# Optimization experiments

Measured on AMD Instinct MI355X. Metric: run time of the kernel, lower is better.

Reference implementation:

```python
import jax, jax.numpy as jnp
import numpy as np

B, S, D = 2, 2048, 1024
H = 16
HD = D // H  # 64
ROPE_BASE = 10000.0


def rotate_half(x):
    x1, x2 = jnp.split(x, 2, axis=-1)
    return jnp.concatenate((-x2, x1), axis=-1)


def rope_cos_sin(seq_len, dim, dtype):
    inv_freq = 1.0 / (ROPE_BASE ** (jnp.arange(0, dim, 2, dtype=jnp.float32) / dim))
    t = jnp.arange(seq_len, dtype=jnp.float32)
    freqs = jnp.einsum('i,j->ij', t, inv_freq)          # [S, dim/2]
    emb = jnp.concatenate((freqs, freqs), axis=-1)      # [S, dim]
    return jnp.cos(emb).astype(dtype), jnp.sin(emb).astype(dtype)


def setup_inputs() -> dict:
    key = jax.random.key(0)
    ks = jax.random.split(key, 5)
    std = 0.02
    return {
        'x': jax.random.normal(ks[0], (B, S, D), dtype=jnp.float32),
        'wq': jax.random.normal(ks[1], (D, D), dtype=jnp.float32) * std,
        'wk': jax.random.normal(ks[2], (D, D), dtype=jnp.float32) * std,
        'wv': jax.random.normal(ks[3], (D, D), dtype=jnp.float32) * std,
        'wo': jax.random.normal(ks[4], (D, D), dtype=jnp.float32) * std,
    }


def reference(x, wq, wk, wv, wo):
    b, s, d = x.shape
    # Q/K/V projections (nn.Linear: x @ W.T)
    q = jnp.einsum('bsd,ed->bse', x, wq).reshape(b, s, H, HD).transpose(0, 2, 1, 3)
    k = jnp.einsum('bsd,ed->bse', x, wk).reshape(b, s, H, HD).transpose(0, 2, 1, 3)
    v = jnp.einsum('bsd,ed->bse', x, wv).reshape(b, s, H, HD).transpose(0, 2, 1, 3)
    # RoPE
    cos, sin = rope_cos_sin(s, HD, x.dtype)  # [s, HD]
    cos = cos[None, None]  # [1,1,s,HD]
    sin = sin[None, None]
    q = q * cos + rotate_half(q) * sin
    k = k * cos + rotate_half(k) * sin
    # Causal SDPA
    scale = HD ** -0.5
    scores = jnp.einsum('bhqd,bhkd->bhqk', q, k) * scale
    causal = jnp.tril(jnp.ones((s, s), dtype=bool))
    scores = jnp.where(causal[None, None], scores, jnp.finfo(scores.dtype).min)
    attn = jax.nn.softmax(scores, axis=-1)
    out = jnp.einsum('bhqk,bhkd->bhqd', attn, v)
    out = out.transpose(0, 2, 1, 3).reshape(b, s, d)
    return jnp.einsum('bsd,ed->bse', out, wo)
```

## Files before the change

### kernel.cpp

```cpp
#include <hip/hip_runtime.h>
#include <hip/hip_bf16.h>
#include <cstdint>
#include <cstddef>

#define BDIM 2
#define SDIM 2048
#define DDIM 1024
#define HN   16
#define HDIM 64

using bf16 = __bf16;
typedef __attribute__((ext_vector_type(8))) __bf16 bf16x8;
typedef __attribute__((ext_vector_type(4))) __bf16 bf16x4;
typedef __attribute__((ext_vector_type(4))) float  f32x4;

#define MFMA16(a, b, c) __builtin_amdgcn_mfma_f32_16x16x32_bf16((a), (b), (c), 0, 0, 0)

#define ASYNC16(g, l)                                                          \
  __builtin_amdgcn_global_load_lds(                                            \
      (const __attribute__((address_space(1))) void*)(g),                      \
      (__attribute__((address_space(3))) void*)(l), 16, 0, 0)

#define QSCALE 0.1803368801111204f

__global__ __launch_bounds__(256) void cvt_bf16(const float* __restrict__ src,
                                                bf16* __restrict__ dst, int n4) {
  int i = blockIdx.x * 256 + threadIdx.x;
  if (i < n4) {
    float4 v = ((const float4*)src)[i];
    bf16x4 o = {(__bf16)v.x, (__bf16)v.y, (__bf16)v.z, (__bf16)v.w};
    *(bf16x4*)(dst + (size_t)i * 4) = o;
  }
}

struct Ptr4 { const float* p[4]; };
__global__ __launch_bounds__(256) void cvt_w(Ptr4 srcs, bf16* __restrict__ dst) {
  const int seg = blockIdx.y;
  const float* src = srcs.p[seg];
  int i = blockIdx.x * 256 + threadIdx.x;
  float4 v = ((const float4*)src)[i];
  bf16x4 o = {(__bf16)v.x, (__bf16)v.y, (__bf16)v.z, (__bf16)v.w};
  *(bf16x4*)(dst + (size_t)seg * (DDIM * DDIM) + (size_t)i * 4) = o;
}

__global__ __launch_bounds__(256) void rope_table(float* __restrict__ cosT,
                                                  float* __restrict__ sinT) {
  int i = blockIdx.x * 256 + threadIdx.x;
  int s = i >> 5, j = i & 31;
  float inv = powf(10000.f, -(float)j * (1.f / 32.f));
  float a = (float)s * inv;
  float sn, c;
  sincosf(a, &sn, &c);
  cosT[s * 64 + j]      = c;
  cosT[s * 64 + j + 32] = c;
  sinT[s * 64 + j]      = sn;
  sinT[s * 64 + j + 32] = sn;
}

__global__ __launch_bounds__(256) void fixup_qk(bf16* __restrict__ q,
                                                bf16* __restrict__ k,
                                                const float* __restrict__ cosT,
                                                const float* __restrict__ sinT) {
  const int bh = blockIdx.y;
  const int s = blockIdx.x * 32 + (threadIdx.x >> 3);
  const int j0 = (threadIdx.x & 7) * 4;
  const size_t base = ((size_t)bh * SDIM + s) * HDIM;
  const float4 c4 = *(const float4*)(cosT + s * 64 + j0);
  const float4 s4 = *(const float4*)(sinT + s * 64 + j0);
  const float cc[4] = {c4.x, c4.y, c4.z, c4.w};
  const float ss[4] = {s4.x, s4.y, s4.z, s4.w};

  bf16x4 qlo = *(bf16x4*)(q + base + j0);
  bf16x4 qhi = *(bf16x4*)(q + base + j0 + 32);
  bf16x4 klo = *(bf16x4*)(k + base + j0);
  bf16x4 khi = *(bf16x4*)(k + base + j0 + 32);
  bf16x4 rql, rqh, rkl, rkh;
#pragma unroll
  for (int e = 0; e < 4; ++e) {
    float a = (float)qlo[e], b = (float)qhi[e];
    rql[e] = (__bf16)((a * cc[e] - b * ss[e]) * QSCALE);
    rqh[e] = (__bf16)((b * cc[e] + a * ss[e]) * QSCALE);
    a = (float)klo[e]; b = (float)khi[e];
    rkl[e] = (__bf16)(a * cc[e] - b * ss[e]);
    rkh[e] = (__bf16)(b * cc[e] + a * ss[e]);
  }
  *(bf16x4*)(q + base + j0)      = rql;
  *(bf16x4*)(q + base + j0 + 32) = rqh;
  *(bf16x4*)(k + base + j0)      = rkl;
  *(bf16x4*)(k + base + j0 + 32) = rkh;
}

__global__ __launch_bounds__(512) void gemm_qkv(const bf16* __restrict__ A,
                                                const bf16* __restrict__ Bw,
                                                bf16* __restrict__ C0,
                                                bf16* __restrict__ Vt) {
  constexpr int K = 1024;
  __shared__ __align__(16) bf16 As[2][256 * 64];
  __shared__ __align__(16) bf16 Bs[2][256 * 64];
  const int tid = threadIdx.x;
  const int l = tid & 63, w = tid >> 6;
  const int wr = w >> 2, wc = w & 3;
  const int lr = l & 15, lg = l >> 4;

  const int bid = blockIdx.x;
  const int swb = (bid & 7) * 24 + (bid >> 3);
  const int mt = swb & 15, nt = swb >> 4;
  const int bm = mt * 256, bn = nt * 256;

  f32x4 acc[8][4] = {};

  auto stage = [&](int buf, int k0) {
#pragma unroll
    for (int i = 0; i < 4; ++i) {
      int lin = i * 4096 + tid * 8;
      int row = lin >> 6, col = lin & 63;
      ASYNC16(A + (size_t)(bm + row) * K + (k0 + col), As[buf] + lin);
      ASYNC16(Bw + (size_t)(bn + row) * K + (k0 + col), Bs[buf] + lin);
    }
  };

  stage(0, 0);
  asm volatile("s_waitcnt vmcnt(0)" ::: "memory");
  __builtin_amdgcn_s_barrier();

  for (int k = 0; k < 16; ++k) {
    const int cur = k & 1;
    if (k < 15) {
      stage(cur ^ 1, (k + 1) * 64);
      asm volatile("s_waitcnt vmcnt(8)" ::: "memory");
    } else {
      asm volatile("s_waitcnt vmcnt(0)" ::: "memory");
    }
    __builtin_amdgcn_sched_barrier(0);
    __builtin_amdgcn_s_barrier();

    const bf16* Ab = As[cur];
    const bf16* Bb = Bs[cur];
#pragma unroll
    for (int kc = 0; kc < 2; ++kc) {
      bf16x8 a[8], b[4];
#pragma unroll
      for (int m = 0; m < 8; ++m)
        a[m] = *(const bf16x8*)(Ab + (wr * 128 + m * 16 + lr) * 64 + kc * 32 + lg * 8);
#pragma unroll
      for (int n = 0; n < 4; ++n)
        b[n] = *(const bf16x8*)(Bb + (wc * 64 + n * 16 + lr) * 64 + kc * 32 + lg * 8);
      __builtin_amdgcn_s_setprio(1);
#pragma unroll
      for (int m = 0; m < 8; ++m)
#pragma unroll
        for (int n = 0; n < 4; ++n)
          acc[m][n] = MFMA16(a[m], b[n], acc[m][n]);
      __builtin_amdgcn_s_setprio(0);
    }
    __builtin_amdgcn_sched_barrier(0);
    __builtin_amdgcn_s_barrier();
    __builtin_amdgcn_sched_barrier(0);
  }

  const int z = bn >> 10;
  const int bcol = bn & 1023;
  if (z < 2) {
    bf16* C = C0 + (size_t)z * ((size_t)BDIM * SDIM * DDIM);
#pragma unroll
    for (int m = 0; m < 8; ++m) {
      const int row0 = bm + wr * 128 + m * 16 + lg * 4;
      const int bb = row0 >> 11, s = row0 & (SDIM - 1);
#pragma unroll
      for (int n = 0; n < 4; ++n) {
        const int h = (bcol >> 6) + wc;
        const int hd = n * 16 + lr;
        const size_t base = ((size_t)(bb * HN + h) * SDIM + s) * HDIM + hd;
#pragma unroll
        for (int r = 0; r < 4; ++r)
          C[base + (size_t)r * HDIM] = (__bf16)acc[m][n][r];
      }
    }
  } else {
#pragma unroll
    for (int m = 0; m < 8; ++m) {
      const int row0 = bm + wr * 128 + m * 16 + lg * 4;
      const int bb = row0 >> 11, s0 = row0 & (SDIM - 1);
#pragma unroll
      for (int n = 0; n < 4; ++n) {
        const int h = (bcol >> 6) + wc;
        const int hd = n * 16 + lr;
        bf16x4 pv = {(__bf16)acc[m][n][0], (__bf16)acc[m][n][1],
                     (__bf16)acc[m][n][2], (__bf16)acc[m][n][3]};
        *(bf16x4*)(Vt + ((size_t)(bb * HN + h) * HDIM + hd) * SDIM + s0) = pv;
      }
    }
  }
}

__global__ __launch_bounds__(256) void gemm_out(const bf16* __restrict__ A,
                                                const bf16* __restrict__ Bw,
                                                float* __restrict__ C) {
  constexpr int K = 1024;
  __shared__ __align__(16) bf16 As[128 * 64];
  __shared__ __align__(16) bf16 Bs[128 * 64];
  const int tid = threadIdx.x;
  const int l = tid & 63, w = tid >> 6;
  const int wr = w >> 1, wc = w & 1;
  const int lr = l & 15, lg = l >> 4;
  const int bm = blockIdx.y * 128;
  const int bn = blockIdx.x * 128;

  f32x4 acc[4][4] = {};

  for (int k0 = 0; k0 < K; k0 += 64) {
    __syncthreads();
#pragma unroll
    for (int i = 0; i < 4; ++i) {
      int idx = i * 2048 + tid * 8;
      int row = idx >> 6, col = idx & 63;
      ASYNC16(A + (size_t)(bm + row) * K + (k0 + col), As + idx);
      ASYNC16(Bw + (size_t)(bn + row) * K + (k0 + col), Bs + idx);
    }
    __syncthreads();
#pragma unroll
    for (int c = 0; c < 2; ++c) {
      bf16x8 af[4], bfr[4];
#pragma unroll
      for (int m = 0; m < 4; ++m)
        af[m] = *(const bf16x8*)(As + (wr * 64 + m * 16 + lr) * 64 + c * 32 + lg * 8);
#pragma unroll
      for (int n = 0; n < 4; ++n)
        bfr[n] = *(const bf16x8*)(Bs + (wc * 64 + n * 16 + lr) * 64 + c * 32 + lg * 8);
      __builtin_amdgcn_s_setprio(1);
#pragma unroll
      for (int m = 0; m < 4; ++m)
#pragma unroll
        for (int n = 0; n < 4; ++n)
          acc[m][n] = MFMA16(af[m], bfr[n], acc[m][n]);
      __builtin_amdgcn_s_setprio(0);
    }
  }

#pragma unroll
  for (int m = 0; m < 4; ++m)
#pragma unroll
    for (int n = 0; n < 4; ++n)
#pragma unroll
      for (int r = 0; r < 4; ++r) {
        int row = bm + wr * 64 + m * 16 + lg * 4 + r;
        int col = bn + wc * 64 + n * 16 + lr;
        C[(size_t)row * DDIM + col] = acc[m][n][r];
      }
}

__global__ __launch_bounds__(512) void attn_fwd(const bf16* __restrict__ qg,
                                                const bf16* __restrict__ kg,
                                                const bf16* __restrict__ vtg,
                                                bf16* __restrict__ og) {
  __shared__ __align__(16) bf16 Sl[2][3][4096];
  __shared__ __align__(16) bf16 Pl[8][1024];

  const int tid = threadIdx.x;
  const int l = tid & 63, w = tid >> 6;
  const int g = w >> 2, wg = w & 3;
  const int lr = l & 15, lg = l >> 4;
  const int bh = blockIdx.x;
  const int qt = 31 - blockIdx.y;
  const int q0 = qt * 64;
  const size_t hb = (size_t)bh * SDIM * HDIM;
  const bf16* Q  = qg + hb;
  const bf16* Kp = kg + hb;
  const bf16* Vp = vtg + hb;
  const int b = bh >> 4, h = bh & 15;
  bf16* Pw = &Pl[w][0];
  const int swz = lr & 7;

  const int mm0 = 2 * wg, mm1 = 2 * wg + 1;
  const int f0 = mm0 & 3, c0 = mm0 >> 2;
  const int f1 = mm1 & 3, c1 = mm1 >> 2;
  const int lo0 = mm0 * 512 + l * 8;
  const int lo1 = mm1 * 512 + l * 8;
  bf16* const SlG = &Sl[g][0][0];

  bf16x8 qf[2];
#pragma unroll
  for (int c = 0; c < 2; ++c)
    qf[c] = *(const bf16x8*)(Q + (size_t)(q0 + wg * 16 + lr) * HDIM + c * 32 + lg * 8);

  f32x4 o[4] = {};
  float m = -3e38f, lsum = 0.f;

  const int ng   = (qt >= g) ? ((qt - g) >> 1) + 1 : 0;
  const int smax = (qt >> 1) + 1;

  const bf16* kN0 = Kp + (size_t)(f0 * 16 + lr) * HDIM + c0 * 32 + lg * 8 + (size_t)g * 64 * HDIM;
  const bf16* kN1 = Kp + (size_t)(f1 * 16 + lr) * HDIM + c1 * 32 + lg * 8 + (size_t)g * 64 * HDIM;
  const bf16* vN0 = Vp + (size_t)(f0 * 16 + lr) * SDIM + c0 * 32 + lg * 8 + g * 64;
  const bf16* vN1 = Vp + (size_t)(f1 * 16 + lr) * SDIM + c1 * 32 + lg * 8 + g * 64;

  if (ng > 0) {
    ASYNC16(kN0, SlG + 0 * 4096 + lo0); kN0 += 128 * HDIM;
    ASYNC16(kN1, SlG + 0 * 4096 + lo1); kN1 += 128 * HDIM;
    ASYNC16(vN0, SlG + 1 * 4096 + lo0); vN0 += 128;
    ASYNC16(vN1, SlG + 1 * 4096 + lo1); vN1 += 128;
  }
  __syncthreads();

  int ks = 0, vs = 1;
  for (int s = 0; s < smax; ++s) {
    const int t = 2 * s + g;
    const bool act = (s < ng);
    const int kn = 3 - ks - vs;
    const bool hasNext = act && (s + 1 < ng);

    if (hasNext) {
      ASYNC16(kN0, SlG + kn * 4096 + lo0); kN0 += 128 * HDIM;
      ASYNC16(kN1, SlG + kn * 4096 + lo1); kN1 += 128 * HDIM;
    }

    const bool diag = (t == qt);
    const int fLim = diag ? wg : 3;

    f32x4 sc[4] = {};
    if (act) {
      __builtin_amdgcn_s_setprio(1);
#pragma unroll
      for (int c = 0; c < 2; ++c)
#pragma unroll
        for (int f = 0; f < 4; ++f)
          if (f <= fLim) {
            bf16x8 kfr = *(const bf16x8*)(SlG + ks * 4096 + (c * 4 + f) * 512 + l * 8);
            sc[f] = MFMA16(kfr, qf[c], sc[f]);
          }
      __builtin_amdgcn_s_setprio(0);
    }

    __builtin_amdgcn_s_barrier();
    __builtin_amdgcn_sched_barrier(0);

    if (hasNext) {
      ASYNC16(vN0, SlG + ks * 4096 + lo0); vN0 += 128;
      ASYNC16(vN1, SlG + ks * 4096 + lo1); vN1 += 128;
    }

    if (act) {
      if (diag) {
#pragma unroll
        for (int f = 0; f < 4; ++f)
#pragma unroll
          for (int r = 0; r < 4; ++r) {
            if (f > wg)
              sc[f][r] = -3e38f;
            else if (f == wg)
              sc[f][r] = (lg * 4 + r <= lr) ? sc[f][r] : -3e38f;
          }
      }

      float mxl = -3e38f;
#pragma unroll
      for (int f = 0; f < 4; ++f)
#pragma unroll
        for (int r = 0; r < 4; ++r) mxl = fmaxf(mxl, sc[f][r]);

      if (!__all(mxl - m <= 8.f)) {
        float mx = fmaxf(mxl, __shfl_xor(mxl, 16));
        mx = fmaxf(mx, __shfl_xor(mx, 32));
        float mnew = fmaxf(m, mx);
        float corr = exp2f(m - mnew);
        m = mnew;
        lsum *= corr;
        float cb[4];
#pragma unroll
        for (int r = 0; r < 4; ++r) cb[r] = __shfl(corr, lg * 4 + r);
#pragma unroll
        for (int n = 0; n < 4; ++n)
#pragma unroll
          for (int r = 0; r < 4; ++r) o[n][r] *= cb[r];
      }

      float rs = 0.f;
#pragma unroll
      for (int f = 0; f < 4; ++f) {
        float p0 = exp2f(sc[f][0] - m);
        float p1 = exp2f(sc[f][1] - m);
        float p2 = exp2f(sc[f][2] - m);
        float p3 = exp2f(sc[f][3] - m);
        rs += (p0 + p1) + (p2 + p3);
        bf16x4 pv = {(__bf16)p0, (__bf16)p1, (__bf16)p2, (__bf16)p3};
        const int ch = f * 2 + (lg >> 1);
        *(bf16x4*)(Pw + lr * 64 + ((ch ^ swz) << 3) + (lg & 1) * 4) = pv;
      }
      lsum += rs;

      const int cLim = diag ? (wg >> 1) : 1;
      __builtin_amdgcn_s_setprio(1);
#pragma unroll
      for (int c = 0; c < 2; ++c)
        if (c <= cLim) {
          bf16x8 pf = *(const bf16x8*)(Pw + lr * 64 + (((c * 4 + lg) ^ swz) << 3));
#pragma unroll
          for (int n = 0; n < 4; ++n) {
            bf16x8 vfr = *(const bf16x8*)(SlG + vs * 4096 + (c * 4 + n) * 512 + l * 8);
            o[n] = MFMA16(pf, vfr, o[n]);
          }
        }
      __builtin_amdgcn_s_setprio(0);
    }

    __syncthreads();
    vs = ks;
    ks = kn;
  }

  float* Osh = (float*)&Sl[0][0][0];
  float* Msh = Osh + 4096;
  float* Lsh = Msh + 256;

  if (g == 1) {
    Msh[wg * 64 + l] = m;
    Lsh[wg * 64 + l] = lsum;
#pragma unroll
    for (int n = 0; n < 4; ++n)
#pragma unroll
      for (int r = 0; r < 4; ++r)
        Osh[((wg * 4 + n) * 4 + r) * 64 + l] = o[n][r];
  }
  __syncthreads();

  if (g == 0) {
    float m1 = Msh[wg * 64 + l], l1 = Lsh[wg * 64 + l];
    float mt = fmaxf(m, m1);
    float a0 = exp2f(m - mt), a1 = exp2f(m1 - mt);
    float lt = lsum * a0 + l1 * a1;
    lt += __shfl_xor(lt, 16);
    lt += __shfl_xor(lt, 32);
    float a0b[4], a1b[4], ltb[4];
#pragma unroll
    for (int r = 0; r < 4; ++r) {
      a0b[r] = __shfl(a0, lg * 4 + r);
      a1b[r] = __shfl(a1, lg * 4 + r);
      ltb[r] = __shfl(lt, lg * 4 + r);
    }
#pragma unroll
    for (int r = 0; r < 4; ++r) {
      float rl = 1.f / ltb[r];
      int qr = q0 + 16 * wg + lg * 4 + r;
#pragma unroll
      for (int n = 0; n < 4; ++n) {
        float o1 = Osh[((wg * 4 + n) * 4 + r) * 64 + l];
        og[((size_t)(b * SDIM + qr)) * DDIM + h * HDIM + n * 16 + lr] =
            (__bf16)((o[n][r] * a0b[r] + o1 * a1b[r]) * rl);
      }
    }
  }
}

extern "C" void kernel_launch(void* const* d_in, const int* in_sizes, int n_in,
                              void* d_out, int out_size, void* d_ws, size_t ws_size,
                              hipStream_t stream) {
  const float* x  = (const float*)d_in[0];
  const float* wq = (const float*)d_in[1];
  const float* wk = (const float*)d_in[2];
  const float* wv = (const float*)d_in[3];
  const float* wo = (const float*)d_in[4];

  char* ws = (char*)d_ws;
  const size_t MB = 1024 * 1024;
  bf16* xb   = (bf16*)(ws + 0);
  bf16* wqb  = (bf16*)(ws + 8 * MB);
  bf16* wob  = (bf16*)(ws + 14 * MB);
  bf16* qb   = (bf16*)(ws + 16 * MB);
  bf16* kb   = (bf16*)(ws + 24 * MB);
  bf16* vtb  = (bf16*)(ws + 32 * MB);
  bf16* ob   = (bf16*)(ws + 40 * MB);
  float* cosT = (float*)(ws + 48 * MB);
  float* sinT = (float*)(ws + 49 * MB);

  const int NX = BDIM * SDIM * DDIM;
  const int NW = DDIM * DDIM;

  cvt_bf16<<<NX / 4 / 256, 256, 0, stream>>>(x, xb, NX / 4);
  Ptr4 wsrc{{wq, wk, wv, wo}};
  cvt_w<<<dim3(NW / 4 / 256, 4), 256, 0, stream>>>(wsrc, wqb);
  rope_table<<<(SDIM * 32) / 256, 256, 0, stream>>>(cosT, sinT);
  gemm_qkv<<<192, 512, 0, stream>>>(xb, wqb, qb, vtb);
  fixup_qk<<<dim3(SDIM / 32, 32), 256, 0, stream>>>(qb, kb, cosT, sinT);
  attn_fwd<<<dim3(32, 32), 512, 0, stream>>>(qb, kb, vtb, ob);
  gemm_out<<<dim3(8, 32), 256, 0, stream>>>(ob, wob, (float*)d_out);
}
```

Baseline: 146.9 us.

## Retile QKV GEMM to 128x128 blocks, merge conversion kernels, widen gemm_out blocks

Replaces the double-buffered 256x256 QKV GEMM (192 blocks, 512 threads) with a simpler single-buffered 128x128 tile over a 3D grid (768 blocks, 256 threads), one z-slice per Q/K/V weight. The goal is to fill all compute units, since 192 blocks cannot. The trade is lost load/compute overlap and less data reuse per tile. The input and weight fp32-to-bf16 conversions are fused into one launch, and gemm_out moves to 512 threads with a smaller per-wave tile.

```diff
diff --git a/kernel.cpp b/kernel.cpp
--- a/kernel.cpp
+++ b/kernel.cpp
@@ -23,24 +23,29 @@
 
 #define QSCALE 0.1803368801111204f
 
-__global__ __launch_bounds__(256) void cvt_bf16(const float* __restrict__ src,
-                                                bf16* __restrict__ dst, int n4) {
+struct Ptr5 { const float* p[5]; };
+__global__ __launch_bounds__(256) void cvt_all(Ptr5 srcs, bf16* __restrict__ xb,
+                                               bf16* __restrict__ wb) {
+  const int NX4 = (BDIM * SDIM * DDIM) / 4;
   int i = blockIdx.x * 256 + threadIdx.x;
-  if (i < n4) {
-    float4 v = ((const float4*)src)[i];
-    bf16x4 o = {(__bf16)v.x, (__bf16)v.y, (__bf16)v.z, (__bf16)v.w};
-    *(bf16x4*)(dst + (size_t)i * 4) = o;
-  }
-}
-
-struct Ptr4 { const float* p[4]; };
-__global__ __launch_bounds__(256) void cvt_w(Ptr4 srcs, bf16* __restrict__ dst) {
-  const int seg = blockIdx.y;
-  const float* src = srcs.p[seg];
-  int i = blockIdx.x * 256 + threadIdx.x;
-  float4 v = ((const float4*)src)[i];
+  const float* src;
+  bf16* dst;
+  int j;
+  if (i < NX4) {
+    src = srcs.p[0]; dst = xb; j = i;
+  } else {
+    int k = i - NX4;
+    int seg = k >> 18;
+    j = k & 262143;
+    src = srcs.p[seg + 1];
+    dst = wb + (size_t)seg * (DDIM * DDIM) / 1;
+    dst += 0;
+    j = j;
+    dst = wb + (size_t)seg * (DDIM * DDIM);
+  }
+  float4 v = ((const float4*)src)[j];
   bf16x4 o = {(__bf16)v.x, (__bf16)v.y, (__bf16)v.z, (__bf16)v.w};
-  *(bf16x4*)(dst + (size_t)seg * (DDIM * DDIM) + (size_t)i * 4) = o;
+  *(bf16x4*)(dst + (size_t)j * 4) = o;
 }
 
 __global__ __launch_bounds__(256) void rope_table(float* __restrict__ cosT,
@@ -90,101 +95,75 @@
   *(bf16x4*)(k + base + j0 + 32) = rkh;
 }
 
-__global__ __launch_bounds__(512) void gemm_qkv(const bf16* __restrict__ A,
-                                                const bf16* __restrict__ Bw,
+__global__ __launch_bounds__(256) void gemm_qkv(const bf16* __restrict__ A,
+                                                const bf16* __restrict__ B0,
                                                 bf16* __restrict__ C0,
                                                 bf16* __restrict__ Vt) {
   constexpr int K = 1024;
-  __shared__ __align__(16) bf16 As[2][256 * 64];
-  __shared__ __align__(16) bf16 Bs[2][256 * 64];
+  __shared__ __align__(16) bf16 As[128 * 64];
+  __shared__ __align__(16) bf16 Bs[128 * 64];
   const int tid = threadIdx.x;
   const int l = tid & 63, w = tid >> 6;
-  const int wr = w >> 2, wc = w & 3;
+  const int wr = w >> 1, wc = w & 1;
   const int lr = l & 15, lg = l >> 4;
-
-  const int bid = blockIdx.x;
-  const int swb = (bid & 7) * 24 + (bid >> 3);
-  const int mt = swb & 15, nt = swb >> 4;
-  const int bm = mt * 256, bn = nt * 256;
-
-  f32x4 acc[8][4] = {};
-
-  auto stage = [&](int buf, int k0) {
+  const int bm = blockIdx.y * 128;
+  const int bn = blockIdx.x * 128;
+  const bf16* Bw = B0 + (size_t)blockIdx.z * (1024 * 1024);
+
+  f32x4 acc[4][4] = {};
+
+  for (int k0 = 0; k0 < K; k0 += 64) {
+    __syncthreads();
 #pragma unroll
     for (int i = 0; i < 4; ++i) {
-      int lin = i * 4096 + tid * 8;
-      int row = lin >> 6, col = lin & 63;
-      ASYNC16(A + (size_t)(bm + row) * K + (k0 + col), As[buf] + lin);
-      ASYNC16(Bw + (size_t)(bn + row) * K + (k0 + col), Bs[buf] + lin);
-    }
-  };
-
-  stage(0, 0);
-  asm volatile("s_waitcnt vmcnt(0)" ::: "memory");
-  __builtin_amdgcn_s_barrier();
-
-  for (int k = 0; k < 16; ++k) {
-    const int cur = k & 1;
-    if (k < 15) {
-      stage(cur ^ 1, (k + 1) * 64);
-      asm volatile("s_waitcnt vmcnt(8)" ::: "memory");
-    } else {
-      asm volatile("s_waitcnt vmcnt(0)" ::: "memory");
-    }
-    __builtin_amdgcn_sched_barrier(0);
-    __builtin_amdgcn_s_barrier();
-
-    const bf16* Ab = As[cur];
-    const bf16* Bb = Bs[cur];
-#pragma unroll
-    for (int kc = 0; kc < 2; ++kc) {
-      bf16x8 a[8], b[4];
-#pragma unroll
-      for (int m = 0; m < 8; ++m)
-        a[m] = *(const bf16x8*)(Ab + (wr * 128 + m * 16 + lr) * 64 + kc * 32 + lg * 8);
+      int idx = i * 2048 + tid * 8;
+      int row = idx >> 6, col = idx & 63;
+      ASYNC16(A + (size_t)(bm + row) * K + (k0 + col), As + idx);
+      ASYNC16(Bw + (size_t)(bn + row) * K + (k0 + col), Bs + idx);
+    }
+    __syncthreads();
+#pragma unroll
+    for (int c = 0; c < 2; ++c) {
+      bf16x8 af[4], bfr[4];
+#pragma unroll
+      for (int m = 0; m < 4; ++m)
+        af[m] = *(const bf16x8*)(As + (wr * 64 + m * 16 + lr) * 64 + c * 32 + lg * 8);
 #pragma unroll
       for (int n = 0; n < 4; ++n)
-        b[n] = *(const bf16x8*)(Bb + (wc * 64 + n * 16 + lr) * 64 + kc * 32 + lg * 8);
+        bfr[n] = *(const bf16x8*)(Bs + (wc * 64 + n * 16 + lr) * 64 + c * 32 + lg * 8);
       __builtin_amdgcn_s_setprio(1);
 #pragma unroll
-      for (int m = 0; m < 8; ++m)
+      for (int m = 0; m < 4; ++m)
 #pragma unroll
         for (int n = 0; n < 4; ++n)
-          acc[m][n] = MFMA16(a[m], b[n], acc[m][n]);
+          acc[m][n] = MFMA16(af[m], bfr[n], acc[m][n]);
       __builtin_amdgcn_s_setprio(0);
     }
-    __builtin_amdgcn_sched_barrier(0);
-    __builtin_amdgcn_s_barrier();
-    __builtin_amdgcn_sched_barrier(0);
-  }
-
-  const int z = bn >> 10;
-  const int bcol = bn & 1023;
+  }
+
+  const int z = blockIdx.z;
   if (z < 2) {
     bf16* C = C0 + (size_t)z * ((size_t)BDIM * SDIM * DDIM);
 #pragma unroll
-    for (int m = 0; m < 8; ++m) {
-      const int row0 = bm + wr * 128 + m * 16 + lg * 4;
-      const int bb = row0 >> 11, s = row0 & (SDIM - 1);
+    for (int m = 0; m < 4; ++m)
+#pragma unroll
+      for (int n = 0; n < 4; ++n)
+#pragma unroll
+        for (int r = 0; r < 4; ++r) {
+          int row = bm + wr * 64 + m * 16 + lg * 4 + r;
+          int col = bn + wc * 64 + n * 16 + lr;
+          size_t off = (((size_t)(row >> 11) * HN + (col >> 6)) * SDIM + (row & (SDIM - 1))) * HDIM + (col & 63);
+          C[off] = (__bf16)acc[m][n][r];
+        }
+  } else {
+#pragma unroll
+    for (int m = 0; m < 4; ++m) {
+      const int row0 = bm + wr * 64 + m * 16 + lg * 4;
+      const int bb = row0 >> 11, s0 = row0 & (SDIM - 1);
 #pragma unroll
       for (int n = 0; n < 4; ++n) {
-        const int h = (bcol >> 6) + wc;
-        const int hd = n * 16 + lr;
-        const size_t base = ((size_t)(bb * HN + h) * SDIM + s) * HDIM + hd;
-#pragma unroll
-        for (int r = 0; r < 4; ++r)
-          C[base + (size_t)r * HDIM] = (__bf16)acc[m][n][r];
-      }
-    }
-  } else {
-#pragma unroll
-    for (int m = 0; m < 8; ++m) {
-      const int row0 = bm + wr * 128 + m * 16 + lg * 4;
-      const int bb = row0 >> 11, s0 = row0 & (SDIM - 1);
-#pragma unroll
-      for (int n = 0; n < 4; ++n) {
-        const int h = (bcol >> 6) + wc;
-        const int hd = n * 16 + lr;
+        const int col = bn + wc * 64 + n * 16 + lr;
+        const int h = col >> 6, hd = col & 63;
         bf16x4 pv = {(__bf16)acc[m][n][0], (__bf16)acc[m][n][1],
                      (__bf16)acc[m][n][2], (__bf16)acc[m][n][3]};
         *(bf16x4*)(Vt + ((size_t)(bb * HN + h) * HDIM + hd) * SDIM + s0) = pv;
@@ -193,7 +172,7 @@
   }
 }
 
-__global__ __launch_bounds__(256) void gemm_out(const bf16* __restrict__ A,
+__global__ __launch_bounds__(512) void gemm_out(const bf16* __restrict__ A,
                                                 const bf16* __restrict__ Bw,
                                                 float* __restrict__ C) {
   constexpr int K = 1024;
@@ -206,13 +185,13 @@
   const int bm = blockIdx.y * 128;
   const int bn = blockIdx.x * 128;
 
-  f32x4 acc[4][4] = {};
+  f32x4 acc[2][4] = {};
 
   for (int k0 = 0; k0 < K; k0 += 64) {
     __syncthreads();
 #pragma unroll
-    for (int i = 0; i < 4; ++i) {
-      int idx = i * 2048 + tid * 8;
+    for (int i = 0; i < 2; ++i) {
+      int idx = i * 4096 + tid * 8;
       int row = idx >> 6, col = idx & 63;
       ASYNC16(A + (size_t)(bm + row) * K + (k0 + col), As + idx);
       ASYNC16(Bw + (size_t)(bn + row) * K + (k0 + col), Bs + idx);
@@ -220,16 +199,16 @@
     __syncthreads();
 #pragma unroll
     for (int c = 0; c < 2; ++c) {
-      bf16x8 af[4], bfr[4];
-#pragma unroll
-      for (int m = 0; m < 4; ++m)
-        af[m] = *(const bf16x8*)(As + (wr * 64 + m * 16 + lr) * 64 + c * 32 + lg * 8);
+      bf16x8 af[2], bfr[4];
+#pragma unroll
+      for (int m = 0; m < 2; ++m)
+        af[m] = *(const bf16x8*)(As + (wr * 32 + m * 16 + lr) * 64 + c * 32 + lg * 8);
 #pragma unroll
       for (int n = 0; n < 4; ++n)
         bfr[n] = *(const bf16x8*)(Bs + (wc * 64 + n * 16 + lr) * 64 + c * 32 + lg * 8);
       __builtin_amdgcn_s_setprio(1);
 #pragma unroll
-      for (int m = 0; m < 4; ++m)
+      for (int m = 0; m < 2; ++m)
 #pragma unroll
         for (int n = 0; n < 4; ++n)
           acc[m][n] = MFMA16(af[m], bfr[n], acc[m][n]);
@@ -238,12 +217,12 @@
   }
 
 #pragma unroll
-  for (int m = 0; m < 4; ++m)
+  for (int m = 0; m < 2; ++m)
 #pragma unroll
     for (int n = 0; n < 4; ++n)
 #pragma unroll
       for (int r = 0; r < 4; ++r) {
-        int row = bm + wr * 64 + m * 16 + lg * 4 + r;
+        int row = bm + wr * 32 + m * 16 + lg * 4 + r;
         int col = bn + wc * 64 + n * 16 + lr;
         C[(size_t)row * DDIM + col] = acc[m][n][r];
       }
@@ -475,12 +454,11 @@
   const int NX = BDIM * SDIM * DDIM;
   const int NW = DDIM * DDIM;
 
-  cvt_bf16<<<NX / 4 / 256, 256, 0, stream>>>(x, xb, NX / 4);
-  Ptr4 wsrc{{wq, wk, wv, wo}};
-  cvt_w<<<dim3(NW / 4 / 256, 4), 256, 0, stream>>>(wsrc, wqb);
+  Ptr5 srcs{{x, wq, wk, wv, wo}};
+  cvt_all<<<(NX / 4 + NW) / 256, 256, 0, stream>>>(srcs, xb, wqb);
   rope_table<<<(SDIM * 32) / 256, 256, 0, stream>>>(cosT, sinT);
-  gemm_qkv<<<192, 512, 0, stream>>>(xb, wqb, qb, vtb);
+  gemm_qkv<<<dim3(8, 32, 3), 256, 0, stream>>>(xb, wqb, qb, vtb);
   fixup_qk<<<dim3(SDIM / 32, 32), 256, 0, stream>>>(qb, kb, cosT, sinT);
   attn_fwd<<<dim3(32, 32), 512, 0, stream>>>(qb, kb, vtb, ob);
-  gemm_out<<<dim3(8, 32), 256, 0, stream>>>(ob, wob, (float*)d_out);
-}
+  gemm_out<<<dim3(8, 32), 512, 0, stream>>>(ob, wob, (float*)d_out);
+}
```

Measured after the change: 131.5 us. 1.12x faster.
